# Kernel optimization log

Measured on AMD Instinct MI355X. Metric: run time of the kernel, lower is better.

## Reference

```python
import jax, jax.numpy as jnp
import numpy as np

N_A = 50000
N_B = 50000
E = 500000
D = 128


def setup_inputs() -> dict:
    key = jax.random.key(0)
    ks = jax.random.split(key, 16)
    s = 0.02
    inp = {
        "x_a": jax.random.normal(ks[0], (N_A, D), jnp.float32),
        "x_b": jax.random.normal(ks[1], (N_B, D), jnp.float32),
        # shared GraphEdgeWeight params
        "Wp": jax.random.normal(ks[2], (D, D), jnp.float32) * s,
        "bp": jnp.zeros((D,), jnp.float32),
        "Wc": jax.random.normal(ks[3], (D, D), jnp.float32) * s,
        "bc": jnp.zeros((D,), jnp.float32),
        "W1": jax.random.normal(ks[4], (D, 3 * D), jnp.float32) * s,
        "b1": jnp.zeros((D,), jnp.float32),
        "W2": jax.random.normal(ks[5], (1, D), jnp.float32) * s,
        "b2": jnp.zeros((1,), jnp.float32),
        # GraphConv params for edge type A->B
        "Wrel_ab": jax.random.normal(ks[6], (D, D), jnp.float32) * s,
        "brel_ab": jnp.zeros((D,), jnp.float32),
        "Wroot_ab": jax.random.normal(ks[7], (D, D), jnp.float32) * s,
        "broot_ab": jnp.zeros((D,), jnp.float32),
        # GraphConv params for edge type B->A
        "Wrel_ba": jax.random.normal(ks[8], (D, D), jnp.float32) * s,
        "brel_ba": jnp.zeros((D,), jnp.float32),
        "Wroot_ba": jax.random.normal(ks[9], (D, D), jnp.float32) * s,
        "broot_ba": jnp.zeros((D,), jnp.float32),
        # edge indices: row0 = src node ids, row1 = dst node ids
        "ei_ab": jax.random.randint(ks[10], (2, E), 0, N_A),
        "ei_ba": jax.random.randint(ks[11], (2, E), 0, N_B),
    }
    return inp


def _edge_type_conv(x_src, x_dst, ei, Wp, bp, Wc, bc, W1, b1, W2, b2,
                    Wrel, brel, Wroot, broot, n_dst):
    # gather endpoint features per edge  [E, D]
    par = x_src[ei[0]]
    cld = x_dst[ei[1]]
    # GraphEdgeWeight: encoders (Linear + LeakyReLU; dropout inactive in eval)
    ep = jax.nn.leaky_relu(par @ Wp.T + bp, negative_slope=0.01)
    ec = jax.nn.leaky_relu(cld @ Wc.T + bc, negative_slope=0.01)
    feat = jnp.concatenate([ep, ec, jnp.abs(par - cld)], axis=-1)  # [E, 3D]
    h = jax.nn.relu(feat @ W1.T + b1)                              # [E, D]
    w = jax.nn.sigmoid(h @ W2.T + b2)[:, 0]                        # [E]
    # GraphConv: out_i = Wrel @ sum_{j->i} w_e x_j + Wroot @ x_i (+ biases)
    msg = jax.ops.segment_sum(par * w[:, None], ei[1], num_segments=n_dst)
    return msg @ Wrel.T + brel + x_dst @ Wroot.T + broot


def reference(x_a, x_b, Wp, bp, Wc, bc, W1, b1, W2, b2,
              Wrel_ab, brel_ab, Wroot_ab, broot_ab,
              Wrel_ba, brel_ba, Wroot_ba, broot_ba,
              ei_ab, ei_ba):
    out_b = _edge_type_conv(x_a, x_b, ei_ab, Wp, bp, Wc, bc, W1, b1, W2, b2,
                            Wrel_ab, brel_ab, Wroot_ab, broot_ab, N_B)
    out_a = _edge_type_conv(x_b, x_a, ei_ba, Wp, bp, Wc, bc, W1, b1, W2, b2,
                            Wrel_ba, brel_ba, Wroot_ba, broot_ba, N_A)
    return out_a, out_b
```

## Files before the change

### kernel.cpp

```cpp
#include <hip/hip_runtime.h>
#include <hip/hip_bf16.h>

typedef unsigned short u16;
typedef __attribute__((ext_vector_type(8))) short bf16x8;
typedef __attribute__((ext_vector_type(2))) short s16x2;
typedef __attribute__((ext_vector_type(4))) float f32x4;

#define N_NODES 50000
#define EDGES 500000
#define WPT 31250
#define EPB 2048
#define EPW (EPB * 4)
#define NWAVES 3125
#define NBLK 782

__device__ __forceinline__ u16 f2bf(float f) {
  return __builtin_bit_cast(u16, __float2bfloat16(f));
}
__device__ __forceinline__ float bf2f(u16 u) {
  return __builtin_bit_cast(float, ((unsigned)u) << 16);
}
__device__ __forceinline__ float bfe(bf16x8 v, int j) {
  return bf2f((u16)v[j]);
}

__device__ __forceinline__ void pk_atomic_bf16(u16* addr, float lo, float hi) {
#if __has_builtin(__builtin_amdgcn_global_atomic_fadd_v2bf16)
  s16x2 v;
  v[0] = (short)f2bf(lo);
  v[1] = (short)f2bf(hi);
  __builtin_amdgcn_global_atomic_fadd_v2bf16(
      (__attribute__((address_space(1))) s16x2*)addr, v);
#else
  unsigned* p = (unsigned*)addr;
  unsigned old = *p, assumed;
  do {
    assumed = old;
    float l2 = bf2f((u16)(assumed & 0xffff)) + lo;
    float h2 = bf2f((u16)(assumed >> 16)) + hi;
    unsigned nv = (unsigned)f2bf(l2) | ((unsigned)f2bf(h2) << 16);
    old = atomicCAS(p, assumed, nv);
  } while (old != assumed);
#endif
}

__global__ __launch_bounds__(256) void prep_weights_zero(
    const float* __restrict__ Wp, const float* __restrict__ Wc,
    const float* __restrict__ W1,
    const float* __restrict__ Wrel_ab, const float* __restrict__ Wroot_ab,
    const float* __restrict__ Wrel_ba, const float* __restrict__ Wroot_ba,
    u16* __restrict__ out, u16* __restrict__ msg)
{
  if (blockIdx.x >= 576) {
    size_t t = (size_t)(blockIdx.x - 576) * 256 + threadIdx.x;
    bf16x8 z = {0, 0, 0, 0, 0, 0, 0, 0};
    *(bf16x8*)(msg + t * 8) = z;
    return;
  }
  int tid = blockIdx.x * 256 + threadIdx.x;
  int m = tid >> 14;
  int idx = tid & 16383;
  int r = idx >> 7;
  int c = idx & 127;
  float val;
  switch (m) {
    case 0: val = Wp[r * 128 + c]; break;
    case 1: val = Wc[r * 128 + c]; break;
    case 2: val = W1[r * 384 + c]; break;
    case 3: val = W1[r * 384 + 128 + c]; break;
    case 4: val = W1[r * 384 + 256 + c]; break;
    case 5: val = Wrel_ab[r * 128 + c]; break;
    case 6: val = Wroot_ab[r * 128 + c]; break;
    case 7: val = Wrel_ba[r * 128 + c]; break;
    default: val = Wroot_ba[r * 128 + c]; break;
  }
  out[tid] = f2bf(val);
}

__global__ __launch_bounds__(256) void encoder2(
    const float* __restrict__ xa, const float* __restrict__ xb,
    const u16* __restrict__ Wp_b, const float* __restrict__ bp,
    const u16* __restrict__ Wc_b, const float* __restrict__ bc,
    const u16* __restrict__ W1a_b, const float* __restrict__ b1,
    const u16* __restrict__ W1b_b,
    u16* __restrict__ xa_bf, u16* __restrict__ xb_bf,
    u16* __restrict__ u_a, u16* __restrict__ v_a,
    u16* __restrict__ u_b, u16* __restrict__ v_b)
{
  __shared__ u16 tile[4][2176];
  int widx = threadIdx.x >> 6;
  int w = blockIdx.x * 4 + widx;
  int type = (w >= NBLK * 4) ? 1 : 0;
  int nw = w - type * NBLK * 4;
  if (nw >= NWAVES) nw = NWAVES - 1;
  const float* x = type ? xb : xa;
  u16* xbf_out = type ? xb_bf : xa_bf;
  u16* u_out = type ? u_b : u_a;
  u16* v_out = type ? v_b : v_a;
  int row0 = nw * 16;
  int lane = threadIdx.x & 63;
  int col = lane & 15;
  int quad = lane >> 4;
  u16* tl = tile[widx];

  bf16x8 af[4];
#pragma unroll
  for (int ks = 0; ks < 4; ks++) {
    const float* xp = x + (size_t)(row0 + col) * 128 + ks * 32 + quad * 8;
    f32x4 lo = *(const f32x4*)xp;
    f32x4 hi = *(const f32x4*)(xp + 4);
    bf16x8 o;
#pragma unroll
    for (int j = 0; j < 4; j++) {
      o[j]     = (short)f2bf(lo[j]);
      o[j + 4] = (short)f2bf(hi[j]);
    }
    af[ks] = o;
    *(bf16x8*)(xbf_out + (size_t)(row0 + col) * 128 + ks * 32 + quad * 8) = o;
  }

  f32x4 zero = {0.f, 0.f, 0.f, 0.f};

  for (int chain = 0; chain < 2; chain++) {
    const u16* Wenc = chain ? Wc_b : Wp_b;
    const float* benc = chain ? bc : bp;
    const u16* Wmix = chain ? W1b_b : W1a_b;
    const float* bmix = chain ? nullptr : b1;
    u16* outp = chain ? v_out : u_out;

    f32x4 acc[8];
#pragma unroll
    for (int nt = 0; nt < 8; nt++) acc[nt] = zero;
#pragma unroll
    for (int ks = 0; ks < 4; ks++) {
      const u16* wp = Wenc + col * 128 + ks * 32 + quad * 8;
#pragma unroll
      for (int nt = 0; nt < 8; nt++) {
        bf16x8 bf = *(const bf16x8*)(wp + nt * 2048);
        acc[nt] = __builtin_amdgcn_mfma_f32_16x16x32_bf16(af[ks], bf, acc[nt], 0, 0, 0);
      }
    }
#pragma unroll
    for (int nt = 0; nt < 8; nt++) {
      float be = benc[nt * 16 + col];
#pragma unroll
      for (int r = 0; r < 4; r++) {
        float v = acc[nt][r] + be;
        v = v > 0.f ? v : 0.01f * v;
        tl[(quad * 4 + r) * 136 + nt * 16 + col] = f2bf(v);
      }
    }
    bf16x8 a2[4];
#pragma unroll
    for (int ks = 0; ks < 4; ks++)
      a2[ks] = *(const bf16x8*)&tl[col * 136 + ks * 32 + quad * 8];

    f32x4 acc2[8];
#pragma unroll
    for (int nt = 0; nt < 8; nt++) acc2[nt] = zero;
#pragma unroll
    for (int ks = 0; ks < 4; ks++) {
      const u16* wp = Wmix + col * 128 + ks * 32 + quad * 8;
#pragma unroll
      for (int nt = 0; nt < 8; nt++) {
        bf16x8 bf = *(const bf16x8*)(wp + nt * 2048);
        acc2[nt] = __builtin_amdgcn_mfma_f32_16x16x32_bf16(a2[ks], bf, acc2[nt], 0, 0, 0);
      }
    }
#pragma unroll
    for (int nt = 0; nt < 8; nt++) {
      float bm = bmix ? bmix[nt * 16 + col] : 0.f;
#pragma unroll
      for (int r = 0; r < 4; r++)
        outp[(size_t)(row0 + quad * 4 + r) * 128 + nt * 16 + col] = f2bf(acc2[nt][r] + bm);
    }
  }
}

__global__ __launch_bounds__(256) void out_gemm2(
    const u16* __restrict__ xa_bf, const u16* __restrict__ xb_bf,
    const u16* __restrict__ msgX_a, const u16* __restrict__ msgX_b,
    const u16* __restrict__ Wrelba_b, const u16* __restrict__ Wrelab_b,
    const u16* __restrict__ Wrootba_b, const u16* __restrict__ Wrootab_b,
    const float* __restrict__ brel_ba, const float* __restrict__ broot_ba,
    const float* __restrict__ brel_ab, const float* __restrict__ broot_ab,
    float* __restrict__ out_a, float* __restrict__ out_b)
{
  int w = blockIdx.x * 4 + (threadIdx.x >> 6);
  int type = (w >= NBLK * 4) ? 1 : 0;
  int nw = w - type * NBLK * 4;
  if (nw >= NWAVES) return;
  const u16* xbf = type ? xb_bf : xa_bf;
  const u16* msg = type ? msgX_b : msgX_a;
  const u16* Wrel = type ? Wrelab_b : Wrelba_b;
  const u16* Wroot = type ? Wrootab_b : Wrootba_b;
  const float* brel = type ? brel_ab : brel_ba;
  const float* broot = type ? broot_ab : broot_ba;
  float* outp = type ? out_b : out_a;
  int row0 = nw * 16;
  int lane = threadIdx.x & 63;
  int col = lane & 15;
  int quad = lane >> 4;

  bf16x8 ax[4], am[4];
#pragma unroll
  for (int ks = 0; ks < 4; ks++) {
    ax[ks] = *(const bf16x8*)(xbf + (size_t)(row0 + col) * 128 + ks * 32 + quad * 8);
    am[ks] = *(const bf16x8*)(msg + (size_t)(row0 + col) * 128 + ks * 32 + quad * 8);
  }

  f32x4 zero = {0.f, 0.f, 0.f, 0.f};
  f32x4 acc[8];
#pragma unroll
  for (int nt = 0; nt < 8; nt++) acc[nt] = zero;
#pragma unroll
  for (int ks = 0; ks < 4; ks++) {
    const u16* wp1 = Wrel + col * 128 + ks * 32 + quad * 8;
    const u16* wp2 = Wroot + col * 128 + ks * 32 + quad * 8;
#pragma unroll
    for (int nt = 0; nt < 8; nt++) {
      bf16x8 b1f = *(const bf16x8*)(wp1 + nt * 2048);
      acc[nt] = __builtin_amdgcn_mfma_f32_16x16x32_bf16(am[ks], b1f, acc[nt], 0, 0, 0);
      bf16x8 b2f = *(const bf16x8*)(wp2 + nt * 2048);
      acc[nt] = __builtin_amdgcn_mfma_f32_16x16x32_bf16(ax[ks], b2f, acc[nt], 0, 0, 0);
    }
  }
#pragma unroll
  for (int nt = 0; nt < 8; nt++) {
    int c = nt * 16 + col;
    float b = brel[c] + broot[c];
#pragma unroll
    for (int r = 0; r < 4; r++)
      outp[(size_t)(row0 + quad * 4 + r) * 128 + c] = acc[nt][r] + b;
  }
}

__global__ __launch_bounds__(256) void edge_fused_p(
    const u16* __restrict__ xs, const u16* __restrict__ xd,
    const int* __restrict__ ei,
    const u16* __restrict__ W1c,
    const u16* __restrict__ uT, const u16* __restrict__ vT,
    const float* __restrict__ W2, const float* __restrict__ b2p,
    u16* __restrict__ msgX)
{
  __shared__ u16 tld[4][2176];
  int widx = threadIdx.x >> 6;
  int wt = blockIdx.x * 4 + widx;
  int lane = threadIdx.x & 63;
  int col = lane & 15;
  int quad = lane >> 4;
  int e4 = lane >> 2;
  int c0 = (lane & 3) * 32;
  u16* tl = tld[widx];
  float b2v = b2p[0];

  for (int g = wt; g < WPT; g += EPW) {
    int e0 = g * 16;

    int si = ei[e0 + col];
    int di = ei[EDGES + e0 + col];
    int s2 = ei[e0 + e4];
    int d2 = ei[EDGES + e0 + e4];

    bf16x8 af[4], d8[4];
#pragma unroll
    for (int ks = 0; ks < 4; ks++) {
      af[ks] = *(const bf16x8*)(xs + (size_t)si * 128 + ks * 32 + quad * 8);
      d8[ks] = *(const bf16x8*)(xd + (size_t)di * 128 + ks * 32 + quad * 8);
    }

    bf16x8 df[4];
#pragma unroll
    for (int ks = 0; ks < 4; ks++)
#pragma unroll
      for (int j = 0; j < 8; j++)
        df[ks][j] = (short)f2bf(__builtin_fabsf(bfe(af[ks], j) - bfe(d8[ks], j)));

    f32x4 zero = {0.f, 0.f, 0.f, 0.f};
    f32x4 acc[8];
#pragma unroll
    for (int nt = 0; nt < 8; nt++) acc[nt] = zero;
#pragma unroll
    for (int ks = 0; ks < 4; ks++) {
      const u16* wp = W1c + col * 128 + ks * 32 + quad * 8;
#pragma unroll
      for (int nt = 0; nt < 8; nt++) {
        bf16x8 bf = *(const bf16x8*)(wp + nt * 2048);
        acc[nt] = __builtin_amdgcn_mfma_f32_16x16x32_bf16(df[ks], bf, acc[nt], 0, 0, 0);
      }
    }

    const u16* urow = uT + (size_t)s2 * 128 + c0;
    const u16* vrow = vT + (size_t)d2 * 128 + c0;
    bf16x8 UU[4], VV[4];
#pragma unroll
    for (int k = 0; k < 4; k++) {
      UU[k] = *(const bf16x8*)(urow + k * 8);
      VV[k] = *(const bf16x8*)(vrow + k * 8);
    }

#pragma unroll
    for (int nt = 0; nt < 8; nt++)
#pragma unroll
      for (int r = 0; r < 4; r++)
        tl[(quad * 4 + r) * 136 + nt * 16 + col] = f2bf(acc[nt][r]);

    const u16* trow = &tl[e4 * 136 + c0];
    float p = 0.f;
#pragma unroll
    for (int k = 0; k < 4; k++) {
      bf16x8 tt = *(const bf16x8*)(trow + k * 8);
      f32x4 w0 = *(const f32x4*)(W2 + c0 + k * 8);
      f32x4 w1 = *(const f32x4*)(W2 + c0 + k * 8 + 4);
#pragma unroll
      for (int j = 0; j < 4; j++) {
        float q0 = bfe(tt, j) + bfe(UU[k], j) + bfe(VV[k], j);
        if (q0 > 0.f) p += q0 * w0[j];
        float q1 = bfe(tt, j + 4) + bfe(UU[k], j + 4) + bfe(VV[k], j + 4);
        if (q1 > 0.f) p += q1 * w1[j];
      }
    }
    p += __shfl_xor(p, 1, 64);
    p += __shfl_xor(p, 2, 64);
    float wgt = 1.f / (1.f + __expf(-(p + b2v)));

#pragma unroll
    for (int ks = 0; ks < 4; ks++)
      *(bf16x8*)&tl[col * 136 + ks * 32 + quad * 8] = af[ks];
#pragma unroll
    for (int r = 0; r < 4; r++) {
      int src_lane = (quad * 4 + r) * 4;
      float wr = __shfl(wgt, src_lane, 64);
      int dr = __shfl(d2, src_lane, 64);
      u16* mrow = msgX + (size_t)dr * 128;
      const u16* xrow = &tl[(quad * 4 + r) * 136];
#pragma unroll
      for (int nt = 0; nt < 4; nt++) {
        int c = nt * 32 + col * 2;
        unsigned xv = *(const unsigned*)(xrow + c);
        pk_atomic_bf16(mrow + c, wr * bf2f((u16)(xv & 0xffff)),
                                 wr * bf2f((u16)(xv >> 16)));
      }
    }
  }
}

extern "C" void kernel_launch(void* const* d_in, const int* in_sizes, int n_in,
                              void* d_out, int out_size, void* d_ws, size_t ws_size,
                              hipStream_t stream) {
  const float* x_a      = (const float*)d_in[0];
  const float* x_b      = (const float*)d_in[1];
  const float* Wp       = (const float*)d_in[2];
  const float* bp       = (const float*)d_in[3];
  const float* Wc       = (const float*)d_in[4];
  const float* bc       = (const float*)d_in[5];
  const float* W1       = (const float*)d_in[6];
  const float* b1       = (const float*)d_in[7];
  const float* W2       = (const float*)d_in[8];
  const float* b2       = (const float*)d_in[9];
  const float* Wrel_ab  = (const float*)d_in[10];
  const float* brel_ab  = (const float*)d_in[11];
  const float* Wroot_ab = (const float*)d_in[12];
  const float* broot_ab = (const float*)d_in[13];
  const float* Wrel_ba  = (const float*)d_in[14];
  const float* brel_ba  = (const float*)d_in[15];
  const float* Wroot_ba = (const float*)d_in[16];
  const float* broot_ba = (const float*)d_in[17];
  const int*   ei_ab    = (const int*)d_in[18];
  const int*   ei_ba    = (const int*)d_in[19];

  char* ws = (char*)d_ws;
  u16* Wb        = (u16*)ws;
  u16* Wp_b      = Wb + 0 * 16384;
  u16* Wc_b      = Wb + 1 * 16384;
  u16* W1a_b     = Wb + 2 * 16384;
  u16* W1b_b     = Wb + 3 * 16384;
  u16* W1c_b     = Wb + 4 * 16384;
  u16* Wrelab_b  = Wb + 5 * 16384;
  u16* Wrootab_b = Wb + 6 * 16384;
  u16* Wrelba_b  = Wb + 7 * 16384;
  u16* Wrootba_b = Wb + 8 * 16384;

  u16* xa_bf   = (u16*)(ws + 1048576);
  u16* xb_bf   = (u16*)(ws + 13848576);
  u16* u_a     = (u16*)(ws + 26648576);
  u16* v_a     = (u16*)(ws + 39448576);
  u16* u_b     = (u16*)(ws + 52248576);
  u16* v_b     = (u16*)(ws + 65048576);
  u16* msgX_a  = (u16*)(ws + 77848576);
  u16* msgX_b  = (u16*)(ws + 90648576);

  float* out_a = (float*)d_out;
  float* out_b = out_a + (size_t)N_NODES * 128;

  prep_weights_zero<<<6826, 256, 0, stream>>>(Wp, Wc, W1, Wrel_ab, Wroot_ab,
                                              Wrel_ba, Wroot_ba, Wb, msgX_a);

  encoder2<<<2 * NBLK, 256, 0, stream>>>(x_a, x_b, Wp_b, bp, Wc_b, bc,
                                         W1a_b, b1, W1b_b,
                                         xa_bf, xb_bf, u_a, v_a, u_b, v_b);

  edge_fused_p<<<EPB, 256, 0, stream>>>(xa_bf, xb_bf, ei_ab, W1c_b,
                                        u_a, v_b, W2, b2, msgX_b);

  edge_fused_p<<<EPB, 256, 0, stream>>>(xb_bf, xa_bf, ei_ba, W1c_b,
                                        u_b, v_a, W2, b2, msgX_a);

  out_gemm2<<<2 * NBLK, 256, 0, stream>>>(xa_bf, xb_bf, msgX_a, msgX_b,
                                          Wrelba_b, Wrelab_b,
                                          Wrootba_b, Wrootab_b,
                                          brel_ba, broot_ba, brel_ab, broot_ab,
                                          out_a, out_b);
}
```

Before: 640.5 us.

## Split encoder chains across waves and overlap root GEMM with edge kernels

Moves the fp32-to-bf16 conversion of node features into the prep kernel. The encoder now assigns each encoder chain (parent or child) to its own wave, doubling the wave count and shortening per-wave work. The root-weight GEMM is computed by extra blocks appended to each edge kernel, which write bias plus root term to the output; the final kernel then only adds the message GEMM with a read-modify-write. The aim is better occupancy and overlap of the dense root GEMM with the atomic-heavy edge phase, at the cost of an extra output read pass and an extra small pass over the inputs.

```diff
diff --git a/kernel.cpp b/kernel.cpp
--- a/kernel.cpp
+++ b/kernel.cpp
@@ -44,13 +44,34 @@
 #endif
 }
 
-__global__ __launch_bounds__(256) void prep_weights_zero(
+__global__ __launch_bounds__(256) void prep_all(
     const float* __restrict__ Wp, const float* __restrict__ Wc,
     const float* __restrict__ W1,
     const float* __restrict__ Wrel_ab, const float* __restrict__ Wroot_ab,
     const float* __restrict__ Wrel_ba, const float* __restrict__ Wroot_ba,
-    u16* __restrict__ out, u16* __restrict__ msg)
+    const float* __restrict__ xa, const float* __restrict__ xb,
+    u16* __restrict__ out, u16* __restrict__ msg,
+    u16* __restrict__ xa_bf, u16* __restrict__ xb_bf)
 {
+  if (blockIdx.x >= 6826) {
+    int t = (blockIdx.x - 6826) * 256 + threadIdx.x;
+    const int HALF = (N_NODES * 128) / 8;
+    const float* src;
+    u16* dst;
+    int idx;
+    if (t < HALF) { src = xa; dst = xa_bf; idx = t * 8; }
+    else          { src = xb; dst = xb_bf; idx = (t - HALF) * 8; }
+    f32x4 a = *(const f32x4*)(src + idx);
+    f32x4 b = *(const f32x4*)(src + idx + 4);
+    bf16x8 o;
+#pragma unroll
+    for (int j = 0; j < 4; j++) {
+      o[j]     = (short)f2bf(a[j]);
+      o[j + 4] = (short)f2bf(b[j]);
+    }
+    *(bf16x8*)(dst + idx) = o;
+    return;
+  }
   if (blockIdx.x >= 576) {
     size_t t = (size_t)(blockIdx.x - 576) * 256 + threadIdx.x;
     bf16x8 z = {0, 0, 0, 0, 0, 0, 0, 0};
@@ -77,26 +98,31 @@
   out[tid] = f2bf(val);
 }
 
-__global__ __launch_bounds__(256) void encoder2(
-    const float* __restrict__ xa, const float* __restrict__ xb,
+__global__ __launch_bounds__(256) void enc_uv(
+    const u16* __restrict__ xa_bf, const u16* __restrict__ xb_bf,
     const u16* __restrict__ Wp_b, const float* __restrict__ bp,
     const u16* __restrict__ Wc_b, const float* __restrict__ bc,
     const u16* __restrict__ W1a_b, const float* __restrict__ b1,
     const u16* __restrict__ W1b_b,
-    u16* __restrict__ xa_bf, u16* __restrict__ xb_bf,
     u16* __restrict__ u_a, u16* __restrict__ v_a,
     u16* __restrict__ u_b, u16* __restrict__ v_b)
 {
   __shared__ u16 tile[4][2176];
   int widx = threadIdx.x >> 6;
   int w = blockIdx.x * 4 + widx;
-  int type = (w >= NBLK * 4) ? 1 : 0;
-  int nw = w - type * NBLK * 4;
-  if (nw >= NWAVES) nw = NWAVES - 1;
-  const float* x = type ? xb : xa;
-  u16* xbf_out = type ? xb_bf : xa_bf;
-  u16* u_out = type ? u_b : u_a;
-  u16* v_out = type ? v_b : v_a;
+  if (w > 12499) w = 12499;
+  int type = w / 6250;
+  int rem = w - type * 6250;
+  int chain = rem / 3125;
+  int nw = rem - chain * 3125;
+
+  const u16* xbf = type ? xb_bf : xa_bf;
+  const u16* Wenc = chain ? Wc_b : Wp_b;
+  const float* benc = chain ? bc : bp;
+  const u16* Wmix = chain ? W1b_b : W1a_b;
+  const float* bmix = chain ? (const float*)nullptr : b1;
+  u16* outp = chain ? (type ? v_b : v_a) : (type ? u_b : u_a);
+
   int row0 = nw * 16;
   int lane = threadIdx.x & 63;
   int col = lane & 15;
@@ -105,109 +131,226 @@
 
   bf16x8 af[4];
 #pragma unroll
+  for (int ks = 0; ks < 4; ks++)
+    af[ks] = *(const bf16x8*)(xbf + (size_t)(row0 + col) * 128 + ks * 32 + quad * 8);
+
+  f32x4 zero = {0.f, 0.f, 0.f, 0.f};
+  f32x4 acc[8];
+#pragma unroll
+  for (int nt = 0; nt < 8; nt++) acc[nt] = zero;
+#pragma unroll
   for (int ks = 0; ks < 4; ks++) {
-    const float* xp = x + (size_t)(row0 + col) * 128 + ks * 32 + quad * 8;
-    f32x4 lo = *(const f32x4*)xp;
-    f32x4 hi = *(const f32x4*)(xp + 4);
-    bf16x8 o;
-#pragma unroll
-    for (int j = 0; j < 4; j++) {
-      o[j]     = (short)f2bf(lo[j]);
-      o[j + 4] = (short)f2bf(hi[j]);
-    }
-    af[ks] = o;
-    *(bf16x8*)(xbf_out + (size_t)(row0 + col) * 128 + ks * 32 + quad * 8) = o;
-  }
+    const u16* wp = Wenc + col * 128 + ks * 32 + quad * 8;
+#pragma unroll
+    for (int nt = 0; nt < 8; nt++) {
+      bf16x8 bf = *(const bf16x8*)(wp + nt * 2048);
+      acc[nt] = __builtin_amdgcn_mfma_f32_16x16x32_bf16(af[ks], bf, acc[nt], 0, 0, 0);
+    }
+  }
+#pragma unroll
+  for (int nt = 0; nt < 8; nt++) {
+    float be = benc[nt * 16 + col];
+#pragma unroll
+    for (int r = 0; r < 4; r++) {
+      float v = acc[nt][r] + be;
+      v = v > 0.f ? v : 0.01f * v;
+      tl[(quad * 4 + r) * 136 + nt * 16 + col] = f2bf(v);
+    }
+  }
+  bf16x8 a2[4];
+#pragma unroll
+  for (int ks = 0; ks < 4; ks++)
+    a2[ks] = *(const bf16x8*)&tl[col * 136 + ks * 32 + quad * 8];
+
+  f32x4 acc2[8];
+#pragma unroll
+  for (int nt = 0; nt < 8; nt++) acc2[nt] = zero;
+#pragma unroll
+  for (int ks = 0; ks < 4; ks++) {
+    const u16* wp = Wmix + col * 128 + ks * 32 + quad * 8;
+#pragma unroll
+    for (int nt = 0; nt < 8; nt++) {
+      bf16x8 bf = *(const bf16x8*)(wp + nt * 2048);
+      acc2[nt] = __builtin_amdgcn_mfma_f32_16x16x32_bf16(a2[ks], bf, acc2[nt], 0, 0, 0);
+    }
+  }
+#pragma unroll
+  for (int nt = 0; nt < 8; nt++) {
+    float bm = bmix ? bmix[nt * 16 + col] : 0.f;
+#pragma unroll
+    for (int r = 0; r < 4; r++)
+      outp[(size_t)(row0 + quad * 4 + r) * 128 + nt * 16 + col] = f2bf(acc2[nt][r] + bm);
+  }
+}
+
+__global__ __launch_bounds__(256) void edge_root(
+    const u16* __restrict__ xs, const u16* __restrict__ xd,
+    const int* __restrict__ ei,
+    const u16* __restrict__ W1c,
+    const u16* __restrict__ uT, const u16* __restrict__ vT,
+    const float* __restrict__ W2, const float* __restrict__ b2p,
+    u16* __restrict__ msgX,
+    const u16* __restrict__ Wroot, const float* __restrict__ brel,
+    const float* __restrict__ broot, float* __restrict__ outp)
+{
+  __shared__ u16 tld[4][2176];
+  int widx = threadIdx.x >> 6;
+  int lane = threadIdx.x & 63;
+  int col = lane & 15;
+  int quad = lane >> 4;
 
   f32x4 zero = {0.f, 0.f, 0.f, 0.f};
 
-  for (int chain = 0; chain < 2; chain++) {
-    const u16* Wenc = chain ? Wc_b : Wp_b;
-    const float* benc = chain ? bc : bp;
-    const u16* Wmix = chain ? W1b_b : W1a_b;
-    const float* bmix = chain ? nullptr : b1;
-    u16* outp = chain ? v_out : u_out;
+  if (blockIdx.x >= EPB) {
+    int nw = (blockIdx.x - EPB) * 4 + widx;
+    if (nw >= NWAVES) return;
+    int row0 = nw * 16;
+
+    bf16x8 ax[4];
+#pragma unroll
+    for (int ks = 0; ks < 4; ks++)
+      ax[ks] = *(const bf16x8*)(xs + (size_t)(row0 + col) * 128 + ks * 32 + quad * 8);
 
     f32x4 acc[8];
 #pragma unroll
     for (int nt = 0; nt < 8; nt++) acc[nt] = zero;
 #pragma unroll
     for (int ks = 0; ks < 4; ks++) {
-      const u16* wp = Wenc + col * 128 + ks * 32 + quad * 8;
+      const u16* wp = Wroot + col * 128 + ks * 32 + quad * 8;
 #pragma unroll
       for (int nt = 0; nt < 8; nt++) {
         bf16x8 bf = *(const bf16x8*)(wp + nt * 2048);
-        acc[nt] = __builtin_amdgcn_mfma_f32_16x16x32_bf16(af[ks], bf, acc[nt], 0, 0, 0);
+        acc[nt] = __builtin_amdgcn_mfma_f32_16x16x32_bf16(ax[ks], bf, acc[nt], 0, 0, 0);
       }
     }
 #pragma unroll
     for (int nt = 0; nt < 8; nt++) {
-      float be = benc[nt * 16 + col];
-#pragma unroll
-      for (int r = 0; r < 4; r++) {
-        float v = acc[nt][r] + be;
-        v = v > 0.f ? v : 0.01f * v;
-        tl[(quad * 4 + r) * 136 + nt * 16 + col] = f2bf(v);
-      }
-    }
-    bf16x8 a2[4];
+      int c = nt * 16 + col;
+      float b = brel[c] + broot[c];
+#pragma unroll
+      for (int r = 0; r < 4; r++)
+        outp[(size_t)(row0 + quad * 4 + r) * 128 + c] = acc[nt][r] + b;
+    }
+    return;
+  }
+
+  int wt = blockIdx.x * 4 + widx;
+  int e4 = lane >> 2;
+  int c0 = (lane & 3) * 32;
+  u16* tl = tld[widx];
+  float b2v = b2p[0];
+
+  for (int g = wt; g < WPT; g += EPW) {
+    int e0 = g * 16;
+
+    int si = ei[e0 + col];
+    int di = ei[EDGES + e0 + col];
+    int s2 = ei[e0 + e4];
+    int d2 = ei[EDGES + e0 + e4];
+
+    bf16x8 af[4], d8[4];
+#pragma unroll
+    for (int ks = 0; ks < 4; ks++) {
+      af[ks] = *(const bf16x8*)(xs + (size_t)si * 128 + ks * 32 + quad * 8);
+      d8[ks] = *(const bf16x8*)(xd + (size_t)di * 128 + ks * 32 + quad * 8);
+    }
+
+    bf16x8 df[4];
 #pragma unroll
     for (int ks = 0; ks < 4; ks++)
-      a2[ks] = *(const bf16x8*)&tl[col * 136 + ks * 32 + quad * 8];
-
-    f32x4 acc2[8];
-#pragma unroll
-    for (int nt = 0; nt < 8; nt++) acc2[nt] = zero;
+#pragma unroll
+      for (int j = 0; j < 8; j++)
+        df[ks][j] = (short)f2bf(__builtin_fabsf(bfe(af[ks], j) - bfe(d8[ks], j)));
+
+    f32x4 acc[8];
+#pragma unroll
+    for (int nt = 0; nt < 8; nt++) acc[nt] = zero;
 #pragma unroll
     for (int ks = 0; ks < 4; ks++) {
-      const u16* wp = Wmix + col * 128 + ks * 32 + quad * 8;
+      const u16* wp = W1c + col * 128 + ks * 32 + quad * 8;
 #pragma unroll
       for (int nt = 0; nt < 8; nt++) {
         bf16x8 bf = *(const bf16x8*)(wp + nt * 2048);
-        acc2[nt] = __builtin_amdgcn_mfma_f32_16x16x32_bf16(a2[ks], bf, acc2[nt], 0, 0, 0);
+        acc[nt] = __builtin_amdgcn_mfma_f32_16x16x32_bf16(df[ks], bf, acc[nt], 0, 0, 0);
       }
     }
-#pragma unroll
-    for (int nt = 0; nt < 8; nt++) {
-      float bm = bmix ? bmix[nt * 16 + col] : 0.f;
+
+    const u16* urow = uT + (size_t)s2 * 128 + c0;
+    const u16* vrow = vT + (size_t)d2 * 128 + c0;
+    bf16x8 UU[4], VV[4];
+#pragma unroll
+    for (int k = 0; k < 4; k++) {
+      UU[k] = *(const bf16x8*)(urow + k * 8);
+      VV[k] = *(const bf16x8*)(vrow + k * 8);
+    }
+
+#pragma unroll
+    for (int nt = 0; nt < 8; nt++)
 #pragma unroll
       for (int r = 0; r < 4; r++)
-        outp[(size_t)(row0 + quad * 4 + r) * 128 + nt * 16 + col] = f2bf(acc2[nt][r] + bm);
-    }
-  }
-}
-
-__global__ __launch_bounds__(256) void out_gemm2(
-    const u16* __restrict__ xa_bf, const u16* __restrict__ xb_bf,
+        tl[(quad * 4 + r) * 136 + nt * 16 + col] = f2bf(acc[nt][r]);
+
+    const u16* trow = &tl[e4 * 136 + c0];
+    float p = 0.f;
+#pragma unroll
+    for (int k = 0; k < 4; k++) {
+      bf16x8 tt = *(const bf16x8*)(trow + k * 8);
+      f32x4 w0 = *(const f32x4*)(W2 + c0 + k * 8);
+      f32x4 w1 = *(const f32x4*)(W2 + c0 + k * 8 + 4);
+#pragma unroll
+      for (int j = 0; j < 4; j++) {
+        float q0 = bfe(tt, j) + bfe(UU[k], j) + bfe(VV[k], j);
+        if (q0 > 0.f) p += q0 * w0[j];
+        float q1 = bfe(tt, j + 4) + bfe(UU[k], j + 4) + bfe(VV[k], j + 4);
+        if (q1 > 0.f) p += q1 * w1[j];
+      }
+    }
+    p += __shfl_xor(p, 1, 64);
+    p += __shfl_xor(p, 2, 64);
+    float wgt = 1.f / (1.f + __expf(-(p + b2v)));
+
+#pragma unroll
+    for (int ks = 0; ks < 4; ks++)
+      *(bf16x8*)&tl[col * 136 + ks * 32 + quad * 8] = af[ks];
+#pragma unroll
+    for (int r = 0; r < 4; r++) {
+      int src_lane = (quad * 4 + r) * 4;
+      float wr = __shfl(wgt, src_lane, 64);
+      int dr = __shfl(d2, src_lane, 64);
+      u16* mrow = msgX + (size_t)dr * 128;
+      const u16* xrow = &tl[(quad * 4 + r) * 136];
+#pragma unroll
+      for (int nt = 0; nt < 4; nt++) {
+        int c = nt * 32 + col * 2;
+        unsigned xv = *(const unsigned*)(xrow + c);
+        pk_atomic_bf16(mrow + c, wr * bf2f((u16)(xv & 0xffff)),
+                                 wr * bf2f((u16)(xv >> 16)));
+      }
+    }
+  }
+}
+
+__global__ __launch_bounds__(256) void out_msg(
     const u16* __restrict__ msgX_a, const u16* __restrict__ msgX_b,
     const u16* __restrict__ Wrelba_b, const u16* __restrict__ Wrelab_b,
-    const u16* __restrict__ Wrootba_b, const u16* __restrict__ Wrootab_b,
-    const float* __restrict__ brel_ba, const float* __restrict__ broot_ba,
-    const float* __restrict__ brel_ab, const float* __restrict__ broot_ab,
     float* __restrict__ out_a, float* __restrict__ out_b)
 {
   int w = blockIdx.x * 4 + (threadIdx.x >> 6);
   int type = (w >= NBLK * 4) ? 1 : 0;
   int nw = w - type * NBLK * 4;
   if (nw >= NWAVES) return;
-  const u16* xbf = type ? xb_bf : xa_bf;
   const u16* msg = type ? msgX_b : msgX_a;
   const u16* Wrel = type ? Wrelab_b : Wrelba_b;
-  const u16* Wroot = type ? Wrootab_b : Wrootba_b;
-  const float* brel = type ? brel_ab : brel_ba;
-  const float* broot = type ? broot_ab : broot_ba;
   float* outp = type ? out_b : out_a;
   int row0 = nw * 16;
   int lane = threadIdx.x & 63;
   int col = lane & 15;
   int quad = lane >> 4;
 
-  bf16x8 ax[4], am[4];
-#pragma unroll
-  for (int ks = 0; ks < 4; ks++) {
-    ax[ks] = *(const bf16x8*)(xbf + (size_t)(row0 + col) * 128 + ks * 32 + quad * 8);
+  bf16x8 am[4];
+#pragma unroll
+  for (int ks = 0; ks < 4; ks++)
     am[ks] = *(const bf16x8*)(msg + (size_t)(row0 + col) * 128 + ks * 32 + quad * 8);
-  }
 
   f32x4 zero = {0.f, 0.f, 0.f, 0.f};
   f32x4 acc[8];
@@ -215,132 +358,20 @@
   for (int nt = 0; nt < 8; nt++) acc[nt] = zero;
 #pragma unroll
   for (int ks = 0; ks < 4; ks++) {
-    const u16* wp1 = Wrel + col * 128 + ks * 32 + quad * 8;
-    const u16* wp2 = Wroot + col * 128 + ks * 32 + quad * 8;
+    const u16* wp = Wrel + col * 128 + ks * 32 + quad * 8;
 #pragma unroll
     for (int nt = 0; nt < 8; nt++) {
-      bf16x8 b1f = *(const bf16x8*)(wp1 + nt * 2048);
-      acc[nt] = __builtin_amdgcn_mfma_f32_16x16x32_bf16(am[ks], b1f, acc[nt], 0, 0, 0);
-      bf16x8 b2f = *(const bf16x8*)(wp2 + nt * 2048);
-      acc[nt] = __builtin_amdgcn_mfma_f32_16x16x32_bf16(ax[ks], b2f, acc[nt], 0, 0, 0);
+      bf16x8 bf = *(const bf16x8*)(wp + nt * 2048);
+      acc[nt] = __builtin_amdgcn_mfma_f32_16x16x32_bf16(am[ks], bf, acc[nt], 0, 0, 0);
     }
   }
 #pragma unroll
   for (int nt = 0; nt < 8; nt++) {
     int c = nt * 16 + col;
-    float b = brel[c] + broot[c];
-#pragma unroll
-    for (int r = 0; r < 4; r++)
-      outp[(size_t)(row0 + quad * 4 + r) * 128 + c] = acc[nt][r] + b;
-  }
-}
-
-__global__ __launch_bounds__(256) void edge_fused_p(
-    const u16* __restrict__ xs, const u16* __restrict__ xd,
-    const int* __restrict__ ei,
-    const u16* __restrict__ W1c,
-    const u16* __restrict__ uT, const u16* __restrict__ vT,
-    const float* __restrict__ W2, const float* __restrict__ b2p,
-    u16* __restrict__ msgX)
-{
-  __shared__ u16 tld[4][2176];
-  int widx = threadIdx.x >> 6;
-  int wt = blockIdx.x * 4 + widx;
-  int lane = threadIdx.x & 63;
-  int col = lane & 15;
-  int quad = lane >> 4;
-  int e4 = lane >> 2;
-  int c0 = (lane & 3) * 32;
-  u16* tl = tld[widx];
-  float b2v = b2p[0];
-
-  for (int g = wt; g < WPT; g += EPW) {
-    int e0 = g * 16;
-
-    int si = ei[e0 + col];
-    int di = ei[EDGES + e0 + col];
-    int s2 = ei[e0 + e4];
-    int d2 = ei[EDGES + e0 + e4];
-
-    bf16x8 af[4], d8[4];
-#pragma unroll
-    for (int ks = 0; ks < 4; ks++) {
-      af[ks] = *(const bf16x8*)(xs + (size_t)si * 128 + ks * 32 + quad * 8);
-      d8[ks] = *(const bf16x8*)(xd + (size_t)di * 128 + ks * 32 + quad * 8);
-    }
-
-    bf16x8 df[4];
-#pragma unroll
-    for (int ks = 0; ks < 4; ks++)
-#pragma unroll
-      for (int j = 0; j < 8; j++)
-        df[ks][j] = (short)f2bf(__builtin_fabsf(bfe(af[ks], j) - bfe(d8[ks], j)));
-
-    f32x4 zero = {0.f, 0.f, 0.f, 0.f};
-    f32x4 acc[8];
-#pragma unroll
-    for (int nt = 0; nt < 8; nt++) acc[nt] = zero;
-#pragma unroll
-    for (int ks = 0; ks < 4; ks++) {
-      const u16* wp = W1c + col * 128 + ks * 32 + quad * 8;
-#pragma unroll
-      for (int nt = 0; nt < 8; nt++) {
-        bf16x8 bf = *(const bf16x8*)(wp + nt * 2048);
-        acc[nt] = __builtin_amdgcn_mfma_f32_16x16x32_bf16(df[ks], bf, acc[nt], 0, 0, 0);
-      }
-    }
-
-    const u16* urow = uT + (size_t)s2 * 128 + c0;
-    const u16* vrow = vT + (size_t)d2 * 128 + c0;
-    bf16x8 UU[4], VV[4];
-#pragma unroll
-    for (int k = 0; k < 4; k++) {
-      UU[k] = *(const bf16x8*)(urow + k * 8);
-      VV[k] = *(const bf16x8*)(vrow + k * 8);
-    }
-
-#pragma unroll
-    for (int nt = 0; nt < 8; nt++)
-#pragma unroll
-      for (int r = 0; r < 4; r++)
-        tl[(quad * 4 + r) * 136 + nt * 16 + col] = f2bf(acc[nt][r]);
-
-    const u16* trow = &tl[e4 * 136 + c0];
-    float p = 0.f;
-#pragma unroll
-    for (int k = 0; k < 4; k++) {
-      bf16x8 tt = *(const bf16x8*)(trow + k * 8);
-      f32x4 w0 = *(const f32x4*)(W2 + c0 + k * 8);
-      f32x4 w1 = *(const f32x4*)(W2 + c0 + k * 8 + 4);
-#pragma unroll
-      for (int j = 0; j < 4; j++) {
-        float q0 = bfe(tt, j) + bfe(UU[k], j) + bfe(VV[k], j);
-        if (q0 > 0.f) p += q0 * w0[j];
-        float q1 = bfe(tt, j + 4) + bfe(UU[k], j + 4) + bfe(VV[k], j + 4);
-        if (q1 > 0.f) p += q1 * w1[j];
-      }
-    }
-    p += __shfl_xor(p, 1, 64);
-    p += __shfl_xor(p, 2, 64);
-    float wgt = 1.f / (1.f + __expf(-(p + b2v)));
-
-#pragma unroll
-    for (int ks = 0; ks < 4; ks++)
-      *(bf16x8*)&tl[col * 136 + ks * 32 + quad * 8] = af[ks];
 #pragma unroll
     for (int r = 0; r < 4; r++) {
-      int src_lane = (quad * 4 + r) * 4;
-      float wr = __shfl(wgt, src_lane, 64);
-      int dr = __shfl(d2, src_lane, 64);
-      u16* mrow = msgX + (size_t)dr * 128;
-      const u16* xrow = &tl[(quad * 4 + r) * 136];
-#pragma unroll
-      for (int nt = 0; nt < 4; nt++) {
-        int c = nt * 32 + col * 2;
-        unsigned xv = *(const unsigned*)(xrow + c);
-        pk_atomic_bf16(mrow + c, wr * bf2f((u16)(xv & 0xffff)),
-                                 wr * bf2f((u16)(xv >> 16)));
-      }
+      size_t idx = (size_t)(row0 + quad * 4 + r) * 128 + c;
+      outp[idx] = outp[idx] + acc[nt][r];
     }
   }
 }
@@ -393,22 +424,22 @@
   float* out_a = (float*)d_out;
   float* out_b = out_a + (size_t)N_NODES * 128;
 
-  prep_weights_zero<<<6826, 256, 0, stream>>>(Wp, Wc, W1, Wrel_ab, Wroot_ab,
-                                              Wrel_ba, Wroot_ba, Wb, msgX_a);
-
-  encoder2<<<2 * NBLK, 256, 0, stream>>>(x_a, x_b, Wp_b, bp, Wc_b, bc,
-                                         W1a_b, b1, W1b_b,
-                                         xa_bf, xb_bf, u_a, v_a, u_b, v_b);
-
-  edge_fused_p<<<EPB, 256, 0, stream>>>(xa_bf, xb_bf, ei_ab, W1c_b,
-                                        u_a, v_b, W2, b2, msgX_b);
-
-  edge_fused_p<<<EPB, 256, 0, stream>>>(xb_bf, xa_bf, ei_ba, W1c_b,
-                                        u_b, v_a, W2, b2, msgX_a);
-
-  out_gemm2<<<2 * NBLK, 256, 0, stream>>>(xa_bf, xb_bf, msgX_a, msgX_b,
-                                          Wrelba_b, Wrelab_b,
-                                          Wrootba_b, Wrootab_b,
-                                          brel_ba, broot_ba, brel_ab, broot_ab,
-                                          out_a, out_b);
-}
+  prep_all<<<13076, 256, 0, stream>>>(Wp, Wc, W1, Wrel_ab, Wroot_ab,
+                                      Wrel_ba, Wroot_ba, x_a, x_b,
+                                      Wb, msgX_a, xa_bf, xb_bf);
+
+  enc_uv<<<3126, 256, 0, stream>>>(xa_bf, xb_bf, Wp_b, bp, Wc_b, bc,
+                                   W1a_b, b1, W1b_b,
+                                   u_a, v_a, u_b, v_b);
+
+  edge_root<<<EPB + NBLK, 256, 0, stream>>>(xa_bf, xb_bf, ei_ab, W1c_b,
+                                            u_a, v_b, W2, b2, msgX_b,
+                                            Wrootba_b, brel_ba, broot_ba, out_a);
+
+  edge_root<<<EPB + NBLK, 256, 0, stream>>>(xb_bf, xa_bf, ei_ba, W1c_b,
+                                            u_b, v_a, W2, b2, msgX_a,
+                                            Wrootab_b, brel_ab, broot_ab, out_b);
+
+  out_msg<<<2 * NBLK, 256, 0, stream>>>(msgX_a, msgX_b,
+                                        Wrelba_b, Wrelab_b, out_a, out_b);
+}
```

After: 663.6 us. 1.04x slower.
